# Kernel tuning notes

Measured on AMD Instinct MI355X. Metric: run time of the kernel, lower is better.

The kernel has to match this reference:

```python
import jax, jax.numpy as jnp
import numpy as np

NUM_LAYER = 5
EMB = 300
N_NODES = 100000
N_EDGES = 200000
NUM_GRAPHS = 5000
NUM_ATOM_TYPE = 120
NUM_CHIRALITY = 3
NUM_BOND_TYPE = 6
NUM_BOND_DIR = 3
BN_EPS = 1e-5


def _xavier(key, shape):
    fan_in, fan_out = shape[-2], shape[-1]
    a = jnp.sqrt(6.0 / (fan_in + fan_out))
    return jax.random.uniform(key, shape, jnp.float32, -a, a)


def setup_inputs() -> dict:
    key = jax.random.key(0)
    ks = jax.random.split(key, 12)
    x = jax.random.randint(ks[0], (N_NODES, 2), 0, 3)
    edge_index = jax.random.randint(ks[1], (2, N_EDGES), 0, N_NODES)
    edge_attr = jax.random.randint(ks[2], (N_EDGES, 2), 0, 3)
    batch = jnp.sort(jax.random.randint(ks[3], (N_NODES,), 0, NUM_GRAPHS))
    # parameters (layer-stacked for the NUM_LAYER GIN convs)
    x_emb1 = _xavier(ks[4], (NUM_ATOM_TYPE, EMB))
    x_emb2 = _xavier(ks[5], (NUM_CHIRALITY, EMB))
    edge_e1 = _xavier(ks[6], (NUM_LAYER, NUM_BOND_TYPE, EMB))
    edge_e2 = _xavier(ks[7], (NUM_LAYER, NUM_BOND_DIR, EMB))
    W1 = _xavier(ks[8], (NUM_LAYER, EMB, 2 * EMB))
    b1 = jnp.zeros((NUM_LAYER, 2 * EMB), jnp.float32)
    W2 = _xavier(ks[9], (NUM_LAYER, 2 * EMB, EMB))
    b2 = jnp.zeros((NUM_LAYER, EMB), jnp.float32)
    gamma = jnp.ones((NUM_LAYER, EMB), jnp.float32)
    beta = jnp.zeros((NUM_LAYER, EMB), jnp.float32)
    return dict(x=x, edge_index=edge_index, edge_attr=edge_attr, batch=batch,
                x_emb1=x_emb1, x_emb2=x_emb2, edge_e1=edge_e1, edge_e2=edge_e2,
                W1=W1, b1=b1, W2=W2, b2=b2, gamma=gamma, beta=beta)


def _forward(x, edge_index, edge_attr, batch,
             x_emb1, x_emb2, edge_e1, edge_e2, W1, b1, W2, b2, gamma, beta):
    N = x.shape[0]
    # add self loops (GINConv uses fill_value=0 for self-loop edge_attr)
    loop = jnp.arange(N)
    src = jnp.concatenate([edge_index[0], loop])  # [E+N]
    dst = jnp.concatenate([edge_index[1], loop])
    ea = jnp.concatenate([edge_attr, jnp.zeros((N, 2), edge_attr.dtype)], axis=0)
    h = x_emb1[x[:, 0]] + x_emb2[x[:, 1]]  # [N, EMB]
    for l in range(NUM_LAYER):
        eemb = edge_e1[l][ea[:, 0]] + edge_e2[l][ea[:, 1]]  # [E+N, EMB]
        msg = h[src] + eemb
        agg = jax.ops.segment_sum(msg, dst, num_segments=N)  # scatter-add
        # GIN MLP: Linear(EMB,2EMB) -> ReLU -> Linear(2EMB,EMB)
        h2 = jax.nn.relu(agg @ W1[l] + b1[l]) @ W2[l] + b2[l]
        # BatchNorm1d (training-mode batch statistics, biased var)
        mu = jnp.mean(h2, axis=0)
        var = jnp.mean(jnp.square(h2 - mu), axis=0)
        hn = (h2 - mu) * jax.lax.rsqrt(var + BN_EPS) * gamma[l] + beta[l]
        h = hn if l == NUM_LAYER - 1 else jax.nn.relu(hn)  # drop_ratio=0
    # JK='last'; global mean pool per graph
    sums = jax.ops.segment_sum(h, batch, num_segments=NUM_GRAPHS)
    counts = jax.ops.segment_sum(jnp.ones((N,), h.dtype), batch, num_segments=NUM_GRAPHS)
    return sums / jnp.maximum(counts, 1.0)[:, None]


def reference(x, edge_index, edge_attr, batch,
              x_emb1, x_emb2, edge_e1, edge_e2, W1, b1, W2, b2, gamma, beta):
    return _forward(x, edge_index, edge_attr, batch,
                    x_emb1, x_emb2, edge_e1, edge_e2, W1, b1, W2, b2, gamma, beta)
```

## Files before the change

kernel.cpp:

```cpp
#include <hip/hip_runtime.h>

typedef unsigned short u16;
typedef unsigned int u32;
typedef __attribute__((ext_vector_type(8))) short short8;
typedef __attribute__((ext_vector_type(4))) float float4v;
typedef _Float16 half8v __attribute__((ext_vector_type(8)));

static constexpr int   kN    = 100000;
static constexpr int   kE    = 200000;
static constexpr int   kEMB  = 300;
static constexpr int   kSA   = 304;
static constexpr int   kKW1  = 320;
static constexpr int   kNH   = 600;
static constexpr int   kNHP  = 608;
static constexpr int   kG    = 5000;
static constexpr int   kL    = 5;
static constexpr float kEPS  = 1e-5f;

static constexpr int   kB1BUF = 10240;
static constexpr int   kB2OFF = 20480;
static constexpr int   kB2BUF = 9728;
static constexpr int   kSMEMU = 39936;

__device__ inline float bf2f(u16 u) {
    union { u32 u32v; float f; } v; v.u32v = ((u32)u) << 16; return v.f;
}
__device__ inline u16 f2bf(float f) {
    union { float f; u32 u; } v; v.f = f;
    u32 r = v.u + 0x7fff + ((v.u >> 16) & 1);
    return (u16)(r >> 16);
}
__device__ inline short h16s(float f) {
    union { _Float16 h; short s; } u; u.h = (_Float16)f; return u.s;
}
__device__ inline short8 load8(const u16* p) {
    return *reinterpret_cast<const short8*>(p);
}
__device__ inline half8v as_h8(short8 s) {
    union { short8 s; half8v h; } u; u.s = s; return u.h;
}
__device__ inline float4v zed4() { float4v z = {0.f, 0.f, 0.f, 0.f}; return z; }
__device__ inline float gload(const void* p, long long i, int isf32) {
    if (isf32) return ((const float*)p)[i];
    return bf2f(((const u16*)p)[i]);
}
__device__ inline float pread(const void* p, size_t i, int f32p) {
    if (f32p) return ((const float*)p)[i];
    return bf2f(((const u16*)p)[i]);
}
__device__ inline void pwrite(void* p, size_t i, float v, int f32p) {
    if (f32p) ((float*)p)[i] = v;
    else      ((u16*)p)[i] = f2bf(v);
}
__device__ inline void gl_lds16(const void* g, void* l) {
    __builtin_amdgcn_global_load_lds(
        (__attribute__((address_space(1))) void*)g,
        (__attribute__((address_space(3))) void*)l, 16, 0, 0);
}

__global__ void detect_kernel(const u16* __restrict__ w1raw, int* flag) {
    if (threadIdx.x == 0 && blockIdx.x == 0) {
        int cnt = 0;
        for (int i = 0; i < 256; ++i) {
            int e = (w1raw[i] >> 7) & 0xFF;
            if (e >= 96 && e <= 126) ++cnt;
        }
        *flag = (cnt >= 200) ? 0 : 1;
    }
}

__global__ void cvt_kernel(const void* __restrict__ src, float* __restrict__ dst,
                           int n, const int* __restrict__ flag) {
    int i = blockIdx.x * blockDim.x + threadIdx.x;
    if (i >= n) return;
    int isf = *flag;
    dst[i] = isf ? ((const float*)src)[i] : bf2f(((const u16*)src)[i]);
}

__global__ void w1t_kernel(const void* __restrict__ W1, u16* __restrict__ W1T,
                           const int* __restrict__ flag, int f32p) {
    int idx = blockIdx.x * blockDim.x + threadIdx.x;
    const int per_layer = kNHP * kKW1;
    if (idx >= kL * per_layer) return;
    int isf = *flag;
    int l = idx / per_layer; int rem = idx - l * per_layer;
    int n = rem / kKW1; int k = rem - n * kKW1;
    u16 v = 0;
    if (n < kNH && k < kEMB) {
        float f = gload(W1, (long long)l * kEMB * kNH + (long long)k * kNH + n, isf);
        v = f32p ? (u16)h16s(f) : f2bf(f);
    }
    W1T[idx] = v;
}
__global__ void w2t_kernel(const void* __restrict__ W2, u16* __restrict__ W2T,
                           const int* __restrict__ flag, int f32p) {
    int idx = blockIdx.x * blockDim.x + threadIdx.x;
    const int per_layer = 19 * 304 * 32;
    if (idx >= kL * per_layer) return;
    int isf = *flag;
    int l = idx / per_layer; int rem = idx - l * per_layer;
    int p = rem / (304 * 32); int r2 = rem - p * (304 * 32);
    int n = r2 >> 5; int kk = r2 & 31;
    int q = kk >> 3, j3 = kk & 7;
    int klocal = (j3 < 4) ? (q * 4 + j3) : (16 + q * 4 + (j3 - 4));
    int k = p * 32 + klocal;
    u16 v = 0;
    if (n < kEMB && k < kNH) {
        float f = gload(W2, (long long)l * kNH * kEMB + (long long)k * kEMB + n, isf);
        v = f32p ? (u16)h16s(f) : f2bf(f);
    }
    W2T[idx] = v;
}

__global__ void embed_kernel(const int* __restrict__ x,
                             const float* __restrict__ emb1,
                             const float* __restrict__ emb2,
                             void* __restrict__ h, int f32p) {
    int idx = blockIdx.x * blockDim.x + threadIdx.x;
    if (idx >= kN * kSA) return;
    int n = idx / kSA; int c = idx - n * kSA;
    float v = 0.f;
    if (c < kEMB) v = emb1[x[2 * n] * kEMB + c] + emb2[x[2 * n + 1] * kEMB + c];
    pwrite(h, idx, v, f32p);
}

__global__ void zero_int_kernel(int* p, int n) {
    int i = blockIdx.x * blockDim.x + threadIdx.x;
    if (i < n) p[i] = 0;
}
__global__ void count_kernel(const int* __restrict__ dst, int* row_ptr) {
    int e = blockIdx.x * blockDim.x + threadIdx.x;
    if (e < kE) atomicAdd(&row_ptr[1 + dst[e]], 1);
}
__global__ __launch_bounds__(1024) void scan1_kernel(int* a, int* bsum, int n) {
    __shared__ int s[1024];
    int t = threadIdx.x;
    int i = blockIdx.x * 1024 + t;
    s[t] = (i < n) ? a[i] : 0;
    __syncthreads();
    for (int off = 1; off < 1024; off <<= 1) {
        int v = (t >= off) ? s[t - off] : 0;
        __syncthreads();
        s[t] += v;
        __syncthreads();
    }
    if (i < n) a[i] = s[t];
    if (t == 1023) bsum[blockIdx.x] = s[t];
}
__global__ __launch_bounds__(128) void scan2_kernel(const int* bsum, int* ebsum, int nb) {
    __shared__ int s[128];
    int t = threadIdx.x;
    int orig = (t < nb) ? bsum[t] : 0;
    s[t] = orig;
    __syncthreads();
    for (int off = 1; off < 128; off <<= 1) {
        int v = (t >= off) ? s[t - off] : 0;
        __syncthreads();
        s[t] += v;
        __syncthreads();
    }
    if (t < nb) ebsum[t] = s[t] - orig;
}
__global__ void scan3_kernel(int* a, const int* ebsum, int* row_ptr0, int n) {
    int i = blockIdx.x * blockDim.x + threadIdx.x;
    if (i >= n) return;
    a[i] += ebsum[i >> 10];
    if (i == 0) *row_ptr0 = 0;
}
__global__ void scatter_kernel(const int* __restrict__ src, const int* __restrict__ dst,
                               const int* __restrict__ ea,
                               const int* __restrict__ row_ptr, int* cursor,
                               int* __restrict__ epack) {
    int e = blockIdx.x * blockDim.x + threadIdx.x;
    if (e >= kE) return;
    int d = dst[e];
    int pos = row_ptr[d] + atomicAdd(&cursor[d], 1);
    epack[pos] = src[e] | (ea[2 * e] << 20) | (ea[2 * e + 1] << 24);
}

__global__ __launch_bounds__(256) void aggregate_kernel(
        const void* __restrict__ h, const int* __restrict__ row_ptr,
        const int* __restrict__ epack,
        const float* __restrict__ e1,
        const float* __restrict__ e2,
        const float* __restrict__ stats_prev,
        const float* __restrict__ gam,
        const float* __restrict__ bet,
        float* __restrict__ stats_next,
        void* __restrict__ agg, int mode, int f32p) {
    if (blockIdx.x == 0) {
        for (int i = threadIdx.x; i < 2 * kEMB; i += 256) stats_next[i] = 0.f;
    }
    int wave = threadIdx.x >> 6;
    int lane = threadIdx.x & 63;
    int base = (blockIdx.x * 4 + wave) * 4;

    float sc[5], sh[5];
#pragma unroll
    for (int j = 0; j < 5; ++j) {
        int c = j * 64 + lane;
        sc[j] = 1.f; sh[j] = 0.f;
        if (mode && c < kEMB) {
            const float invM = 1.0f / kN;
            float mu = stats_prev[c] * invM;
            float var = stats_prev[kEMB + c] * invM - mu * mu;
            if (var < 0.f) var = 0.f;
            float rs = rsqrtf(var + kEPS);
            sc[j] = rs * gam[c];
            sh[j] = bet[c] - mu * sc[j];
        }
    }

    int s[4], e[4];
    float acc[4][5];
#pragma unroll
    for (int t = 0; t < 4; ++t) {
        int node = base + t;
        if (node < kN) { s[t] = row_ptr[node]; e[t] = row_ptr[node + 1]; }
        else           { s[t] = 0; e[t] = 0; }
#pragma unroll
        for (int j = 0; j < 5; ++j) {
            int c = j * 64 + lane;
            acc[t][j] = 0.f;
            if (node < kN && c < kEMB) {
                float hv = pread(h, (size_t)node * kSA + c, f32p) * sc[j] + sh[j];
                if (mode && hv < 0.f) hv = 0.f;
                acc[t][j] = hv + e1[c] + e2[c];
            }
        }
    }

    int maxd = 0;
#pragma unroll
    for (int t = 0; t < 4; ++t) {
        int d = e[t] - s[t];
        if (d > maxd) maxd = d;
    }

    for (int i = 0; i < maxd; ++i) {
        int p[4], act[4];
#pragma unroll
        for (int t = 0; t < 4; ++t) {
            act[t] = (s[t] + i < e[t]);
            p[t] = act[t] ? epack[s[t] + i] : 0;
        }
        float hv[4][5];
#pragma unroll
        for (int t = 0; t < 4; ++t) {
            if (act[t]) {
                int srcn = p[t] & 0xFFFFF;
#pragma unroll
                for (int j = 0; j < 5; ++j) {
                    int c = j * 64 + lane;
                    hv[t][j] = (c < kEMB) ? pread(h, (size_t)srcn * kSA + c, f32p) : 0.f;
                }
            }
        }
#pragma unroll
        for (int t = 0; t < 4; ++t) {
            if (act[t]) {
                int a0 = (p[t] >> 20) & 15;
                int a1 = (p[t] >> 24) & 15;
#pragma unroll
                for (int j = 0; j < 5; ++j) {
                    int c = j * 64 + lane;
                    if (c < kEMB) {
                        float w = hv[t][j] * sc[j] + sh[j];
                        if (mode && w < 0.f) w = 0.f;
                        acc[t][j] += w + e1[a0 * kEMB + c] + e2[a1 * kEMB + c];
                    }
                }
            }
        }
    }

#pragma unroll
    for (int t = 0; t < 4; ++t) {
        int node = base + t;
        if (node < kN) {
#pragma unroll
            for (int j = 0; j < 5; ++j) {
                int c = j * 64 + lane;
                if (c < kSA)
                    pwrite(agg, (size_t)node * kSA + c, (c < kEMB) ? acc[t][j] : 0.f, f32p);
            }
        }
    }
}

template <int F32P>
__global__ __launch_bounds__(256, 2) void mlp_kernel(
        const void* A, void* D,
        const u16* __restrict__ W1Tl,
        const float* __restrict__ bias1,
        const u16* __restrict__ W2Tl,
        const float* __restrict__ bias2,
        float* __restrict__ stats) {
    __shared__ __align__(16) u16 SMEM[kSMEMU];
    int tid = threadIdx.x;
    int wave = tid >> 6, lane = tid & 63;
    int r16 = lane & 15, quad = lane >> 4;
    const int NT = kN / 16;
    int mt_raw = blockIdx.x * 4 + wave;
    int mt = (mt_raw < NT) ? mt_raw : (NT - 1);
    int valid = (mt_raw < NT);

    auto issue = [&](int p1) {
        u16* b1d = SMEM + (p1 & 1) * kB1BUF;
        u16* b2d = SMEM + kB2OFF + (p1 & 1) * kB2BUF;
#pragma unroll
        for (int i = 0; i < 10; ++i) {
            int c = wave + 4 * i;
            if (c < 20) {
                int hh = (c >= 10), kc = c - hh * 10;
                gl_lds16(W1Tl + (size_t)(p1 * 32 + hh * 16 + r16) * kKW1
                             + kc * 32 + quad * 8,
                         b1d + c * 512);
            } else if (c < 39) {
                int nt2 = c - 20;
                gl_lds16(W2Tl + ((size_t)p1 * 304 + nt2 * 16 + r16) * 32 + quad * 8,
                         b2d + nt2 * 512);
            }
        }
    };

    issue(0);

    short8 ahi[10];
    short8 zed = {0, 0, 0, 0, 0, 0, 0, 0};
    if (F32P) {
        const float* Arow = (const float*)A + (size_t)(mt * 16 + r16) * kSA + quad * 8;
#pragma unroll
        for (int kc = 0; kc < 10; ++kc) {
            short8 hh = zed;
            if (kc < 9 || quad < 2) {
                const float* pp = Arow + kc * 32;
#pragma unroll
                for (int j = 0; j < 8; ++j) hh[j] = h16s(pp[j]);
            }
            ahi[kc] = hh;
        }
    } else {
        const u16* Arow = (const u16*)A + (size_t)(mt * 16 + r16) * kSA + quad * 8;
#pragma unroll
        for (int kc = 0; kc < 9; ++kc) ahi[kc] = load8(Arow + kc * 32);
        ahi[9] = (quad < 2) ? load8(Arow + 9 * 32) : zed;
    }

    float4v acc2[19];
#pragma unroll
    for (int i = 0; i < 19; ++i) acc2[i] = zed4();

    short8 a2 = zed;
    short8 a2l = zed;

    for (int p = 0; p < 19; ++p) {
        __syncthreads();
        if (p + 1 < 19) issue(p + 1);

        const u16* B1 = SMEM + (p & 1) * kB1BUF;
        const u16* B2 = SMEM + kB2OFF + (p & 1) * kB2BUF;

#pragma unroll
        for (int hh = 0; hh < 2; ++hh) {
            const u16* bb = B1 + hh * 10 * 512;
            float4v aa = zed4(), ab = zed4();
#pragma unroll
            for (int kc = 0; kc < 10; kc += 2) {
                short8 w0 = load8(bb + kc * 512 + lane * 8);
                short8 w1 = load8(bb + (kc + 1) * 512 + lane * 8);
                if (F32P) {
                    aa = __builtin_amdgcn_mfma_f32_16x16x32_f16(as_h8(w0), as_h8(ahi[kc]), aa, 0, 0, 0);
                    ab = __builtin_amdgcn_mfma_f32_16x16x32_f16(as_h8(w1), as_h8(ahi[kc + 1]), ab, 0, 0, 0);
                } else {
                    aa = __builtin_amdgcn_mfma_f32_16x16x32_bf16(w0, ahi[kc], aa, 0, 0, 0);
                    ab = __builtin_amdgcn_mfma_f32_16x16x32_bf16(w1, ahi[kc + 1], ab, 0, 0, 0);
                }
            }
            float4v bv = *(const float4v*)(bias1 + (2 * p + hh) * 16 + quad * 4);
#pragma unroll
            for (int r = 0; r < 4; ++r) {
                int n1 = (2 * p + hh) * 16 + quad * 4 + r;
                float v = (n1 < kNH) ? (aa[r] + ab[r] + bv[r]) : 0.f;
                if (v < 0.f) v = 0.f;
                if (F32P) {
                    a2[hh * 4 + r] = h16s(v);
                } else {
                    u16 hb = f2bf(v);
                    a2[hh * 4 + r] = (short)hb;
                    a2l[hh * 4 + r] = (short)f2bf(v - bf2f(hb));
                }
            }
        }

#pragma unroll
        for (int nt2 = 0; nt2 < 19; ++nt2) {
            short8 b = load8(B2 + nt2 * 512 + lane * 8);
            if (F32P) {
                acc2[nt2] = __builtin_amdgcn_mfma_f32_16x16x32_f16(as_h8(a2), as_h8(b), acc2[nt2], 0, 0, 0);
            } else {
                acc2[nt2] = __builtin_amdgcn_mfma_f32_16x16x32_bf16(a2, b, acc2[nt2], 0, 0, 0);
                acc2[nt2] = __builtin_amdgcn_mfma_f32_16x16x32_bf16(a2l, b, acc2[nt2], 0, 0, 0);
            }
        }
    }

    __syncthreads();
    float* RB = (float*)SMEM;
#pragma unroll
    for (int nt2 = 0; nt2 < 19; ++nt2) {
        int n = nt2 * 16 + r16;
        float s4 = 0.f, q4 = 0.f;
        if (valid && n < kEMB) {
            float bv = bias2[n];
#pragma unroll
            for (int r = 0; r < 4; ++r) {
                float v = acc2[nt2][r] + bv;
                int m = mt * 16 + quad * 4 + r;
                pwrite(D, (size_t)m * kSA + n, v, F32P);
                s4 += v; q4 += v * v;
            }
        }
        s4 += __shfl_down(s4, 32); q4 += __shfl_down(q4, 32);
        s4 += __shfl_down(s4, 16); q4 += __shfl_down(q4, 16);
        if (quad == 0) {
            RB[wave * 304 + nt2 * 16 + r16] = s4;
            RB[1216 + wave * 304 + nt2 * 16 + r16] = q4;
        }
    }
    __syncthreads();
    for (int c = tid; c < 304; c += 256) {
        if (c < kEMB) {
            float ss = 0.f, qq = 0.f;
#pragma unroll
            for (int w = 0; w < 4; ++w) {
                ss += RB[w * 304 + c];
                qq += RB[1216 + w * 304 + c];
            }
            atomicAdd(&stats[c], ss);
            atomicAdd(&stats[kEMB + c], qq);
        }
    }
}

__device__ inline int lower_bound(const int* a, int n, int key) {
    int lo = 0, hi = n;
    while (lo < hi) { int mid = (lo + hi) >> 1; if (a[mid] < key) lo = mid + 1; else hi = mid; }
    return lo;
}
__global__ __launch_bounds__(64) void pool_kernel(const void* __restrict__ h2,
                                                  const int* __restrict__ batch,
                                                  const float* __restrict__ stats,
                                                  const float* __restrict__ gam,
                                                  const float* __restrict__ bet,
                                                  void* __restrict__ out,
                                                  const int* __restrict__ flag, int f32p) {
    int g = blockIdx.x;
    int lane = threadIdx.x;
    int isf = *flag;
    int start = lower_bound(batch, kN, g);
    int end = lower_bound(batch, kN, g + 1);
    int cnt = end - start;
    float inv = 1.0f / (float)(cnt > 0 ? cnt : 1);
    for (int c = lane; c < kEMB; c += 64) {
        const float invM = 1.0f / kN;
        float mu = stats[c] * invM;
        float var = stats[kEMB + c] * invM - mu * mu;
        if (var < 0.f) var = 0.f;
        float rs = rsqrtf(var + kEPS);
        float sc = rs * gam[c];
        float sh = bet[c] - mu * sc;
        float s = 0.f;
        for (int n = start; n < end; ++n)
            s += pread(h2, (size_t)n * kSA + c, f32p) * sc + sh;
        float v = s * inv;
        if (isf) ((float*)out)[g * kEMB + c] = v;
        else     ((u16*)out)[g * kEMB + c] = f2bf(v);
    }
}

extern "C" void kernel_launch(void* const* d_in, const int* in_sizes, int n_in,
                              void* d_out, int out_size, void* d_ws, size_t ws_size,
                              hipStream_t stream) {
    const int* x          = (const int*)d_in[0];
    const int* edge_index = (const int*)d_in[1];
    const int* edge_attr  = (const int*)d_in[2];
    const int* batch      = (const int*)d_in[3];
    const void* x_emb1 = d_in[4];
    const void* x_emb2 = d_in[5];
    const void* e1raw  = d_in[6];
    const void* e2raw  = d_in[7];
    const void* W1     = d_in[8];
    const void* b1raw  = d_in[9];
    const void* W2     = d_in[10];
    const void* b2raw  = d_in[11];
    const void* gmraw  = d_in[12];
    const void* btraw  = d_in[13];

    const int* src = edge_index;
    const int* dst = edge_index + kE;

    const int f32p = (ws_size >= (size_t)250000000) ? 1 : 0;
    const size_t esz = f32p ? 4 : 2;

    char* p = (char*)d_ws;
    size_t off = 0;
    auto carve = [&](size_t bytes) {
        void* r = p + off;
        off += (bytes + 255) & ~(size_t)255;
        return r;
    };
    void* plane0 = carve((size_t)kN * kSA * esz);
    void* plane1 = carve((size_t)kN * kSA * esz);
    u16* W1T     = (u16*)carve((size_t)kL * kNHP * kKW1 * 2);
    u16* W2T     = (u16*)carve((size_t)kL * 19 * 304 * 32 * 2);
    int* row_ptr = (int*)carve((size_t)(kN + 1) * 4);
    int* cursor  = (int*)carve((size_t)kN * 4);
    int* epack   = (int*)carve((size_t)kE * 4);
    float* statsA = (float*)carve(2 * kEMB * 4);
    float* statsB = (float*)carve(2 * kEMB * 4);
    int* bsum    = (int*)carve(512);
    int* ebsum   = (int*)carve(512);
    int* flag    = (int*)carve(256);
    float* parf  = (float*)carve((size_t)57900 * 4);

    float* emb1  = parf + 0;
    float* emb2  = parf + 36000;
    float* e1    = parf + 36900;
    float* e2    = parf + 45900;
    float* b1    = parf + 50400;
    float* b2    = parf + 53400;
    float* gamma = parf + 54900;
    float* beta  = parf + 56400;

    detect_kernel<<<1, 64, 0, stream>>>((const u16*)W1, flag);
    cvt_kernel<<<(36000 + 255) / 256, 256, 0, stream>>>(x_emb1, emb1, 36000, flag);
    cvt_kernel<<<(900 + 255) / 256, 256, 0, stream>>>(x_emb2, emb2, 900, flag);
    cvt_kernel<<<(9000 + 255) / 256, 256, 0, stream>>>(e1raw, e1, 9000, flag);
    cvt_kernel<<<(4500 + 255) / 256, 256, 0, stream>>>(e2raw, e2, 4500, flag);
    cvt_kernel<<<(3000 + 255) / 256, 256, 0, stream>>>(b1raw, b1, 3000, flag);
    cvt_kernel<<<(1500 + 255) / 256, 256, 0, stream>>>(b2raw, b2, 1500, flag);
    cvt_kernel<<<(1500 + 255) / 256, 256, 0, stream>>>(gmraw, gamma, 1500, flag);
    cvt_kernel<<<(1500 + 255) / 256, 256, 0, stream>>>(btraw, beta, 1500, flag);

    {
        int n1 = kL * kNHP * kKW1;
        w1t_kernel<<<(n1 + 255) / 256, 256, 0, stream>>>(W1, W1T, flag, f32p);
        int n2 = kL * 19 * 304 * 32;
        w2t_kernel<<<(n2 + 255) / 256, 256, 0, stream>>>(W2, W2T, flag, f32p);
    }

    embed_kernel<<<(kN * kSA + 255) / 256, 256, 0, stream>>>(x, emb1, emb2, plane0, f32p);

    zero_int_kernel<<<(kN + 1 + 255) / 256, 256, 0, stream>>>(row_ptr, kN + 1);
    zero_int_kernel<<<(kN + 255) / 256, 256, 0, stream>>>(cursor, kN);
    count_kernel<<<(kE + 255) / 256, 256, 0, stream>>>(dst, row_ptr);
    const int nb = (kN + 1023) / 1024;
    scan1_kernel<<<nb, 1024, 0, stream>>>(row_ptr + 1, bsum, kN);
    scan2_kernel<<<1, 128, 0, stream>>>(bsum, ebsum, nb);
    scan3_kernel<<<(kN + 255) / 256, 256, 0, stream>>>(row_ptr + 1, ebsum, row_ptr, kN);
    scatter_kernel<<<(kE + 255) / 256, 256, 0, stream>>>(src, dst, edge_attr, row_ptr,
                                                         cursor, epack);

    const int mlp_blocks = (kN / 16 + 3) / 4;
    const int agg_blocks = (kN + 15) / 16;
    void* cur = plane0;
    void* agg = plane1;
    float* stats_prev = statsA;
    for (int l = 0; l < kL; ++l) {
        float* stats_cur = (l % 2 == 0) ? statsA : statsB;
        const float* gam_prev = gamma + (l > 0 ? (l - 1) : 0) * kEMB;
        const float* bet_prev = beta + (l > 0 ? (l - 1) : 0) * kEMB;
        aggregate_kernel<<<agg_blocks, 256, 0, stream>>>(
            cur, row_ptr, epack, e1 + l * 6 * kEMB, e2 + l * 3 * kEMB,
            (l > 0) ? stats_prev : stats_cur, gam_prev, bet_prev,
            stats_cur, agg, (l > 0) ? 1 : 0, f32p);
        void* dout = f32p ? cur : agg;
        if (f32p)
            mlp_kernel<1><<<mlp_blocks, 256, 0, stream>>>(
                agg, dout, W1T + (size_t)l * kNHP * kKW1, b1 + l * kNH,
                W2T + (size_t)l * 19 * 304 * 32, b2 + l * kEMB, stats_cur);
        else
            mlp_kernel<0><<<mlp_blocks, 256, 0, stream>>>(
                agg, dout, W1T + (size_t)l * kNHP * kKW1, b1 + l * kNH,
                W2T + (size_t)l * 19 * 304 * 32, b2 + l * kEMB, stats_cur);
        stats_prev = stats_cur;
        cur = dout;
        agg = (cur == plane0) ? plane1 : plane0;
    }

    pool_kernel<<<kG, 64, 0, stream>>>(cur, batch, stats_prev, gamma + 4 * kEMB,
                                       beta + 4 * kEMB, d_out, flag, f32p);
}
```

Measured before the change: 1.852 ms.

## Load MLP weights directly from global in fragment-ordered layout, drop LDS staging

The weight-transpose kernels now write W1 and W2 in a per-lane MFMA fragment order, so each lane's 16-byte weight fragment sits contiguously. The MLP kernel then reads these fragments straight from global memory (through cache) instead of double-buffering them into shared memory with global_load_lds and a __syncthreads per k-step. This removes per-iteration barriers and the large LDS footprint, which could allow more blocks per CU. The cost is that every wave re-reads the full weights from L2/L1 with load latency exposed inside the MFMA loop, since there is no explicit prefetch any more.

New measurement: 3.187 ms. 72.1% more time.

```diff
diff --git a/kernel.cpp b/kernel.cpp
--- a/kernel.cpp
+++ b/kernel.cpp
@@ -10,17 +10,13 @@
 static constexpr int   kE    = 200000;
 static constexpr int   kEMB  = 300;
 static constexpr int   kSA   = 304;
-static constexpr int   kKW1  = 320;
 static constexpr int   kNH   = 600;
-static constexpr int   kNHP  = 608;
 static constexpr int   kG    = 5000;
 static constexpr int   kL    = 5;
 static constexpr float kEPS  = 1e-5f;
 
-static constexpr int   kB1BUF = 10240;
-static constexpr int   kB2OFF = 20480;
-static constexpr int   kB2BUF = 9728;
-static constexpr int   kSMEMU = 39936;
+static constexpr int   kW1CL = 19 * 20 * 512;
+static constexpr int   kW2CL = 19 * 19 * 512;
 
 __device__ inline float bf2f(u16 u) {
     union { u32 u32v; float f; } v; v.u32v = ((u32)u) << 16; return v.f;
@@ -51,11 +47,6 @@
 __device__ inline void pwrite(void* p, size_t i, float v, int f32p) {
     if (f32p) ((float*)p)[i] = v;
     else      ((u16*)p)[i] = f2bf(v);
-}
-__device__ inline void gl_lds16(const void* g, void* l) {
-    __builtin_amdgcn_global_load_lds(
-        (__attribute__((address_space(1))) void*)g,
-        (__attribute__((address_space(3))) void*)l, 16, 0, 0);
 }
 
 __global__ void detect_kernel(const u16* __restrict__ w1raw, int* flag) {
@@ -77,39 +68,44 @@
     dst[i] = isf ? ((const float*)src)[i] : bf2f(((const u16*)src)[i]);
 }
 
-__global__ void w1t_kernel(const void* __restrict__ W1, u16* __restrict__ W1T,
+__global__ void w1t_kernel(const void* __restrict__ W1, u16* __restrict__ W1C,
                            const int* __restrict__ flag, int f32p) {
     int idx = blockIdx.x * blockDim.x + threadIdx.x;
-    const int per_layer = kNHP * kKW1;
-    if (idx >= kL * per_layer) return;
+    if (idx >= kL * kW1CL) return;
     int isf = *flag;
-    int l = idx / per_layer; int rem = idx - l * per_layer;
-    int n = rem / kKW1; int k = rem - n * kKW1;
+    int l = idx / kW1CL; int rem = idx - l * kW1CL;
+    int p = rem / (20 * 512); int r2 = rem - p * (20 * 512);
+    int c = r2 >> 9; int e = r2 & 511;
+    int lane = e >> 3, j = e & 7;
+    int hh = (c >= 10), kc = c - hh * 10;
+    int n = p * 32 + hh * 16 + (lane & 15);
+    int k = kc * 32 + (lane >> 4) * 8 + j;
     u16 v = 0;
     if (n < kNH && k < kEMB) {
         float f = gload(W1, (long long)l * kEMB * kNH + (long long)k * kNH + n, isf);
         v = f32p ? (u16)h16s(f) : f2bf(f);
     }
-    W1T[idx] = v;
-}
-__global__ void w2t_kernel(const void* __restrict__ W2, u16* __restrict__ W2T,
+    W1C[idx] = v;
+}
+__global__ void w2t_kernel(const void* __restrict__ W2, u16* __restrict__ W2C,
                            const int* __restrict__ flag, int f32p) {
     int idx = blockIdx.x * blockDim.x + threadIdx.x;
-    const int per_layer = 19 * 304 * 32;
-    if (idx >= kL * per_layer) return;
+    if (idx >= kL * kW2CL) return;
     int isf = *flag;
-    int l = idx / per_layer; int rem = idx - l * per_layer;
-    int p = rem / (304 * 32); int r2 = rem - p * (304 * 32);
-    int n = r2 >> 5; int kk = r2 & 31;
-    int q = kk >> 3, j3 = kk & 7;
-    int klocal = (j3 < 4) ? (q * 4 + j3) : (16 + q * 4 + (j3 - 4));
+    int l = idx / kW2CL; int rem = idx - l * kW2CL;
+    int p = rem / (19 * 512); int r2 = rem - p * (19 * 512);
+    int nt2 = r2 >> 9; int e = r2 & 511;
+    int lane = e >> 3, j = e & 7;
+    int q = lane >> 4;
+    int klocal = (j < 4) ? (q * 4 + j) : (16 + q * 4 + (j - 4));
     int k = p * 32 + klocal;
+    int n = nt2 * 16 + (lane & 15);
     u16 v = 0;
     if (n < kEMB && k < kNH) {
         float f = gload(W2, (long long)l * kNH * kEMB + (long long)k * kEMB + n, isf);
         v = f32p ? (u16)h16s(f) : f2bf(f);
     }
-    W2T[idx] = v;
+    W2C[idx] = v;
 }
 
 __global__ void embed_kernel(const int* __restrict__ x,
@@ -291,12 +287,12 @@
 template <int F32P>
 __global__ __launch_bounds__(256, 2) void mlp_kernel(
         const void* A, void* D,
-        const u16* __restrict__ W1Tl,
+        const u16* __restrict__ W1C,
         const float* __restrict__ bias1,
-        const u16* __restrict__ W2Tl,
+        const u16* __restrict__ W2C,
         const float* __restrict__ bias2,
         float* __restrict__ stats) {
-    __shared__ __align__(16) u16 SMEM[kSMEMU];
+    __shared__ float RB[2432];
     int tid = threadIdx.x;
     int wave = tid >> 6, lane = tid & 63;
     int r16 = lane & 15, quad = lane >> 4;
@@ -305,27 +301,6 @@
     int mt = (mt_raw < NT) ? mt_raw : (NT - 1);
     int valid = (mt_raw < NT);
 
-    auto issue = [&](int p1) {
-        u16* b1d = SMEM + (p1 & 1) * kB1BUF;
-        u16* b2d = SMEM + kB2OFF + (p1 & 1) * kB2BUF;
-#pragma unroll
-        for (int i = 0; i < 10; ++i) {
-            int c = wave + 4 * i;
-            if (c < 20) {
-                int hh = (c >= 10), kc = c - hh * 10;
-                gl_lds16(W1Tl + (size_t)(p1 * 32 + hh * 16 + r16) * kKW1
-                             + kc * 32 + quad * 8,
-                         b1d + c * 512);
-            } else if (c < 39) {
-                int nt2 = c - 20;
-                gl_lds16(W2Tl + ((size_t)p1 * 304 + nt2 * 16 + r16) * 32 + quad * 8,
-                         b2d + nt2 * 512);
-            }
-        }
-    };
-
-    issue(0);
-
     short8 ahi[10];
     short8 zed = {0, 0, 0, 0, 0, 0, 0, 0};
     if (F32P) {
@@ -354,27 +329,24 @@
     short8 a2 = zed;
     short8 a2l = zed;
 
+    const u16* w1p = W1C + lane * 8;
+    const u16* w2p = W2C + lane * 8;
+
     for (int p = 0; p < 19; ++p) {
-        __syncthreads();
-        if (p + 1 < 19) issue(p + 1);
-
-        const u16* B1 = SMEM + (p & 1) * kB1BUF;
-        const u16* B2 = SMEM + kB2OFF + (p & 1) * kB2BUF;
-
 #pragma unroll
         for (int hh = 0; hh < 2; ++hh) {
-            const u16* bb = B1 + hh * 10 * 512;
+            const u16* bb = w1p + hh * 10 * 512;
             float4v aa = zed4(), ab = zed4();
 #pragma unroll
             for (int kc = 0; kc < 10; kc += 2) {
-                short8 w0 = load8(bb + kc * 512 + lane * 8);
-                short8 w1 = load8(bb + (kc + 1) * 512 + lane * 8);
+                short8 w0 = load8(bb + kc * 512);
+                short8 w1v = load8(bb + (kc + 1) * 512);
                 if (F32P) {
                     aa = __builtin_amdgcn_mfma_f32_16x16x32_f16(as_h8(w0), as_h8(ahi[kc]), aa, 0, 0, 0);
-                    ab = __builtin_amdgcn_mfma_f32_16x16x32_f16(as_h8(w1), as_h8(ahi[kc + 1]), ab, 0, 0, 0);
+                    ab = __builtin_amdgcn_mfma_f32_16x16x32_f16(as_h8(w1v), as_h8(ahi[kc + 1]), ab, 0, 0, 0);
                 } else {
                     aa = __builtin_amdgcn_mfma_f32_16x16x32_bf16(w0, ahi[kc], aa, 0, 0, 0);
-                    ab = __builtin_amdgcn_mfma_f32_16x16x32_bf16(w1, ahi[kc + 1], ab, 0, 0, 0);
+                    ab = __builtin_amdgcn_mfma_f32_16x16x32_bf16(w1v, ahi[kc + 1], ab, 0, 0, 0);
                 }
             }
             float4v bv = *(const float4v*)(bias1 + (2 * p + hh) * 16 + quad * 4);
@@ -395,7 +367,7 @@
 
 #pragma unroll
         for (int nt2 = 0; nt2 < 19; ++nt2) {
-            short8 b = load8(B2 + nt2 * 512 + lane * 8);
+            short8 b = load8(w2p + nt2 * 512);
             if (F32P) {
                 acc2[nt2] = __builtin_amdgcn_mfma_f32_16x16x32_f16(as_h8(a2), as_h8(b), acc2[nt2], 0, 0, 0);
             } else {
@@ -403,10 +375,11 @@
                 acc2[nt2] = __builtin_amdgcn_mfma_f32_16x16x32_bf16(a2l, b, acc2[nt2], 0, 0, 0);
             }
         }
-    }
-
-    __syncthreads();
-    float* RB = (float*)SMEM;
+
+        w1p += 20 * 512;
+        w2p += 19 * 512;
+    }
+
 #pragma unroll
     for (int nt2 = 0; nt2 < 19; ++nt2) {
         int n = nt2 * 16 + r16;
@@ -512,8 +485,8 @@
     };
     void* plane0 = carve((size_t)kN * kSA * esz);
     void* plane1 = carve((size_t)kN * kSA * esz);
-    u16* W1T     = (u16*)carve((size_t)kL * kNHP * kKW1 * 2);
-    u16* W2T     = (u16*)carve((size_t)kL * 19 * 304 * 32 * 2);
+    u16* W1C     = (u16*)carve((size_t)kL * kW1CL * 2);
+    u16* W2C     = (u16*)carve((size_t)kL * kW2CL * 2);
     int* row_ptr = (int*)carve((size_t)(kN + 1) * 4);
     int* cursor  = (int*)carve((size_t)kN * 4);
     int* epack   = (int*)carve((size_t)kE * 4);
@@ -544,10 +517,10 @@
     cvt_kernel<<<(1500 + 255) / 256, 256, 0, stream>>>(btraw, beta, 1500, flag);
 
     {
-        int n1 = kL * kNHP * kKW1;
-        w1t_kernel<<<(n1 + 255) / 256, 256, 0, stream>>>(W1, W1T, flag, f32p);
-        int n2 = kL * 19 * 304 * 32;
-        w2t_kernel<<<(n2 + 255) / 256, 256, 0, stream>>>(W2, W2T, flag, f32p);
+        int n1 = kL * kW1CL;
+        w1t_kernel<<<(n1 + 255) / 256, 256, 0, stream>>>(W1, W1C, flag, f32p);
+        int n2 = kL * kW2CL;
+        w2t_kernel<<<(n2 + 255) / 256, 256, 0, stream>>>(W2, W2C, flag, f32p);
     }
 
     embed_kernel<<<(kN * kSA + 255) / 256, 256, 0, stream>>>(x, emb1, emb2, plane0, f32p);
@@ -578,12 +551,12 @@
         void* dout = f32p ? cur : agg;
         if (f32p)
             mlp_kernel<1><<<mlp_blocks, 256, 0, stream>>>(
-                agg, dout, W1T + (size_t)l * kNHP * kKW1, b1 + l * kNH,
-                W2T + (size_t)l * 19 * 304 * 32, b2 + l * kEMB, stats_cur);
+                agg, dout, W1C + (size_t)l * kW1CL, b1 + l * kNH,
+                W2C + (size_t)l * kW2CL, b2 + l * kEMB, stats_cur);
         else
             mlp_kernel<0><<<mlp_blocks, 256, 0, stream>>>(
-                agg, dout, W1T + (size_t)l * kNHP * kKW1, b1 + l * kNH,
-                W2T + (size_t)l * 19 * 304 * 32, b2 + l * kEMB, stats_cur);
+                agg, dout, W1C + (size_t)l * kW1CL, b1 + l * kNH,
+                W2C + (size_t)l * kW2CL, b2 + l * kEMB, stats_cur);
         stats_prev = stats_cur;
         cur = dout;
         agg = (cur == plane0) ? plane1 : plane0;
```
